# Kernel tuning notes

Measured on AMD Instinct MI355X. Metric: run time of the kernel, lower is better.

Reference implementation:

```python
import jax, jax.numpy as jnp
from jax import lax
import numpy as np

# ---- init hyperparameters (from init_kwargs) ----
STRIDE = 1
DP_CHANNELS = 1
ATOM_R = 8
ATOM_C = 8
NUMB_ATOM = 128
T_SC = 3
K = 256
BATCH = 32
IMG = 64


def setup_inputs() -> dict:
    key = jax.random.key(0)
    k1, k2 = jax.random.split(key)
    Y = jax.random.normal(k1, (BATCH, DP_CHANNELS, IMG, IMG), dtype=jnp.float32)
    # ConvTranspose2d weight layout: (numb_atom, dp_channels, atom_c, atom_r)
    W = jax.random.normal(k2, (NUMB_ATOM, DP_CHANNELS, ATOM_C, ATOM_R), dtype=jnp.float32)
    # normalise_weights(): each (i, j) filter divided by its L2 norm
    W = W / jnp.sqrt(jnp.sum(W ** 2, axis=(2, 3), keepdims=True))
    return {"Y": Y, "W_D": W}


def _conv_D(X, W):
    # PyTorch ConvTranspose2d (stride=1, no padding): full convolution with
    # spatially-flipped kernel; W is (in=numb_atom, out=dp_channels, kh, kw).
    kh, kw = W.shape[2], W.shape[3]
    return lax.conv_general_dilated(
        X, jnp.flip(W, (2, 3)), (1, 1),
        [(kh - 1, kh - 1), (kw - 1, kw - 1)],
        dimension_numbers=('NCHW', 'IOHW', 'NCHW'))


def _conv_Dt(R, Wt):
    # PyTorch Conv2d (VALID, stride=1): Wt is (out=numb_atom, in=dp, kh, kw)
    return lax.conv_general_dilated(
        R, Wt, (1, 1), 'VALID', dimension_numbers=('NCHW', 'OIHW', 'NCHW'))


def _hard_threshold_k(X, k):
    # keep the k largest-|.| entries per sample (over flattened C,H,W)
    B = X.shape[0]
    flat = X.reshape(B, -1)
    _, idx = lax.top_k(jnp.abs(flat), k)                      # [B, k]
    vals = jnp.take_along_axis(flat, idx, axis=1)             # [B, k]
    out = jnp.zeros_like(flat).at[jnp.arange(B)[:, None], idx].set(vals)
    return out.reshape(X.shape)


def _linesearch(Y, X, W, Wt, k):
    R = Y - _conv_D(X, W)
    g = _conv_Dt(R, Wt)
    l2_start = jnp.sum(R ** 2)

    def attempt(alpha):
        Xu = _hard_threshold_k(X + alpha * g, k)
        err = jnp.sum((Y - _conv_D(Xu, W)) ** 2)
        return Xu, err

    Xu0, err0 = attempt(jnp.float32(1.0))

    def cond(s):
        _, _, err, count = s
        return (err >= l2_start) & (count <= 15)

    def body(s):
        alpha, _, _, count = s
        alpha = alpha * jnp.float32(0.5)
        Xu, err = attempt(alpha)
        return (alpha, Xu, err, count + 1)

    alpha, Xu, err, _ = lax.while_loop(
        cond, body, (jnp.float32(1.0), Xu0, err0, jnp.int32(0)))
    return Xu, err, alpha


def reference(Y, W_D):
    # D_trans.weight = D.weight.permute(0,1,3,2) -> (numb_atom, dp, atom_r, atom_c)
    Wt = jnp.swapaxes(W_D, 2, 3)
    kh, kw = Wt.shape[2], Wt.shape[3]
    B, _, H, W_sp = Y.shape
    X = jnp.zeros((B, W_D.shape[0], H - kh + 1, W_sp - kw + 1), dtype=Y.dtype)
    for _ in range(T_SC):
        X, _, _ = _linesearch(Y, X, W_D, Wt, K)
    return X
```

## Files before the change

kernel.cpp:

```cpp
#include <hip/hip_runtime.h>
#include <stdint.h>

#define NB   32
#define NCH  128
#define IMG  64
#define IMG2 4096
#define OH   57
#define OHW  3249
#define CHW  415872
#define KTOP 256
#define NATT 17
#define NS   32
#define SCAP 512
#define NCAP 1536
#define NBUCK 8192
#define HSHIFT 18
#define TGT  512
#define RSTRIDE 72
#define NZB  257
#define BMW  12996

typedef unsigned long long ull;

__global__ void k_init(int* support_cnt) {
    if (threadIdx.x < NB) support_cnt[threadIdx.x] = 0;
}

__global__ __launch_bounds__(256) void k_resid(
    const float* __restrict__ Y, const float* __restrict__ W,
    const int* __restrict__ support_cnt, const uint32_t* __restrict__ support_idx,
    const float* __restrict__ support_val, float* __restrict__ Rg, double* __restrict__ l2part,
    uint32_t* __restrict__ hist, int* __restrict__ cand_cnt)
{
    int bx = blockIdx.x, tid = threadIdx.x;
    if (bx >= NB) {
        int zb = bx - NB;
        if (zb < 256) {
            ((uint4*)hist)[zb * 256 + tid] = make_uint4(0u, 0u, 0u, 0u);
        } else {
            ((uint4*)cand_cnt)[tid] = make_uint4(0u, 0u, 0u, 0u);
        }
        return;
    }
    int b = bx;
    __shared__ float Rs[IMG2];
    const float4* Y4 = (const float4*)(Y + b * IMG2);
    float4* R4 = (float4*)Rs;
    for (int i = tid; i < IMG2 / 4; i += 256) R4[i] = Y4[i];
    __syncthreads();
    int n = support_cnt[b];
    for (int task = tid; task < n * 64; task += 256) {
        int i = task >> 6, tap = task & 63, p = tap >> 3, q = tap & 7;
        uint32_t idx = support_idx[b * KTOP + i];
        float val = support_val[b * KTOP + i];
        int c = idx / OHW, rem = idx % OHW, s = rem / OH, t = rem % OH;
        float w = W[c * 64 + p * 8 + q];
        atomicAdd(&Rs[(s + p) * IMG + (t + q)], -val * w);
    }
    __syncthreads();
    double acc = 0.0;
    for (int i = tid; i < IMG2; i += 256) {
        float v = Rs[i];
        Rg[b * IMG2 + i] = v;
        acc += (double)v * (double)v;
    }
    __shared__ double red[256];
    red[tid] = acc; __syncthreads();
    for (int s2 = 128; s2 > 0; s2 >>= 1) { if (tid < s2) red[tid] += red[tid + s2]; __syncthreads(); }
    if (tid == 0) l2part[b] = red[0];
}

__global__ __launch_bounds__(256) void k_conv(
    const float* __restrict__ Rg, const float* __restrict__ W,
    float* __restrict__ g_out, uint32_t* __restrict__ hist)
{
    int b = blockIdx.x, cg0 = blockIdx.y, tid = threadIdx.x;
    __shared__ float Rs[71 * 72];
    __shared__ uint32_t hl[NBUCK];
    for (int i = tid; i < 71 * 72; i += 256) Rs[i] = 0.f;
    for (int i = tid; i < NBUCK; i += 256) hl[i] = 0u;
    __syncthreads();
    const float4* R4 = (const float4*)(Rg + b * IMG2);
    for (int i = tid; i < 1024; i += 256) {
        int row = i >> 4, col4 = (i & 15) * 4;
        *(float4*)&Rs[row * 72 + col4] = R4[i];
    }
    __syncthreads();
    int csub = tid >> 7;
    int tile = tid & 127;
    bool active = tile < 120;
    int tr = active ? tile / 15 : 0;
    int tc = active ? tile % 15 : 0;
    int s0 = tr * 8, t0 = tc * 4;

    for (int sub = 0; sub < 4; ++sub) {
        int c = cg0 * 8 + sub * 2 + csub;
        int c_s = __builtin_amdgcn_readfirstlane(c);
        const float* Wc = W + c_s * 64;

        float acc[8][4];
#pragma unroll
        for (int r = 0; r < 8; ++r)
#pragma unroll
            for (int cc = 0; cc < 4; ++cc) acc[r][cc] = 0.f;

#pragma unroll
        for (int rho = 0; rho < 15; ++rho) {
            float rb[12];
            const float* rp = &Rs[(s0 + rho) * 72 + t0];
            *(float4*)&rb[0] = *(const float4*)rp;
            *(float4*)&rb[4] = *(const float4*)(rp + 4);
            *(float4*)&rb[8] = *(const float4*)(rp + 8);
#pragma unroll
            for (int r = 0; r < 8; ++r) {
                const int p = rho - r;
                if (p >= 0 && p < 8) {
#pragma unroll
                    for (int q = 0; q < 8; ++q) {
                        float wv = Wc[q * 8 + p];
#pragma unroll
                        for (int cc = 0; cc < 4; ++cc)
                            acc[r][cc] = fmaf(rb[cc + q], wv, acc[r][cc]);
                    }
                }
            }
        }
        if (active) {
            float* go = g_out + (size_t)(b * NCH + c) * OHW;
#pragma unroll
            for (int r = 0; r < 8; ++r) {
                int s = s0 + r;
                if (s < OH) {
#pragma unroll
                    for (int cc = 0; cc < 4; ++cc) {
                        int t = t0 + cc;
                        if (t < OH) {
                            float v = acc[r][cc];
                            go[s * OH + t] = v;
                            uint32_t bits = __float_as_uint(v) & 0x7fffffffu;
                            atomicAdd(&hl[bits >> HSHIFT], 1u);
                        }
                    }
                }
            }
        }
    }
    __syncthreads();
    for (int i = tid; i < NBUCK; i += 256) {
        uint32_t v = hl[i];
        if (v) atomicAdd(&hist[b * NBUCK + i], v);
    }
}

__global__ __launch_bounds__(256) void k_thresh(const uint32_t* __restrict__ hist,
                                                uint32_t* __restrict__ thr) {
    int b = blockIdx.x, tid = threadIdx.x;
    uint32_t h[32];
    uint32_t s = 0;
    const uint32_t* hb = hist + b * NBUCK + tid * 32;
#pragma unroll
    for (int k = 0; k < 32; ++k) { h[k] = hb[k]; s += h[k]; }
    __shared__ uint32_t buf[2][256];
    int cur = 0;
    buf[0][tid] = s;
    __syncthreads();
    for (int d = 1; d < 256; d <<= 1) {
        uint32_t v = buf[cur][tid];
        if (tid + d < 256) v += buf[cur][tid + d];
        buf[cur ^ 1][tid] = v;
        cur ^= 1;
        __syncthreads();
    }
    uint32_t sufme = buf[cur][tid];
    uint32_t base  = (tid < 255) ? buf[cur][tid + 1] : 0u;
    if (tid == 0 && buf[cur][0] < TGT) thr[b] = 0u;
    if (base < TGT && sufme >= TGT) {
        uint32_t acc = base; int bk = 0;
#pragma unroll
        for (int k = 31; k >= 0; --k) {
            acc += h[k];
            if (acc >= TGT) { bk = tid * 32 + k; break; }
        }
        thr[b] = (uint32_t)bk << HSHIFT;
    }
}

__global__ __launch_bounds__(256) void k_collect(
    const float* __restrict__ g, const uint32_t* __restrict__ thr,
    int* __restrict__ cand_cnt, uint32_t* __restrict__ cand_idx, float* __restrict__ cand_g)
{
    int b = blockIdx.y;
    int i4 = blockIdx.x * 256 + threadIdx.x;
    if (i4 >= CHW / 4) return;
    int slice = blockIdx.x & (NS - 1);
    uint32_t tb = thr[b];
    float4 v4 = ((const float4*)(g + (size_t)b * CHW))[i4];
    float vv[4] = { v4.x, v4.y, v4.z, v4.w };
#pragma unroll
    for (int k = 0; k < 4; ++k) {
        uint32_t bits = __float_as_uint(vv[k]) & 0x7fffffffu;
        if (bits >= tb) {
            int pos = atomicAdd(&cand_cnt[b * NS + slice], 1);
            if (pos < SCAP) {
                cand_idx[(b * NS + slice) * SCAP + pos] = (uint32_t)(i4 * 4 + k);
                cand_g[(b * NS + slice) * SCAP + pos] = vv[k];
            }
        }
    }
}

__global__ __launch_bounds__(1024) void k_suppg(
    const float* __restrict__ g,
    const int* __restrict__ support_cnt, const uint32_t* __restrict__ support_idx,
    const int* __restrict__ cand_cnt, const uint32_t* __restrict__ cand_idx,
    const float* __restrict__ cand_g,
    uint32_t* __restrict__ ns_idx, float* __restrict__ ns_g, uint32_t* __restrict__ ns_pk,
    float* __restrict__ sup_g, uint32_t* __restrict__ sup_pk)
{
    int b = blockIdx.x, tid = threadIdx.x, lane = tid & 63;
    __shared__ uint32_t bm[BMW];
    __shared__ int cnts[NS];
    __shared__ ull ck[NCAP];
    __shared__ float cg_l[NCAP];
    __shared__ int nns_sh;
    int n = support_cnt[b];
    for (int i = tid; i < BMW / 4; i += 1024) ((uint4*)bm)[i] = make_uint4(0u, 0u, 0u, 0u);
    if (tid < NS) cnts[tid] = min(cand_cnt[b * NS + tid], SCAP);
    if (tid == 0) nns_sh = 0;
    __syncthreads();
    if (tid < KTOP) {
        if (tid < n) {
            uint32_t idx = support_idx[b * KTOP + tid];
            atomicOr(&bm[idx >> 5], 1u << (idx & 31));
            float gv = g[(size_t)b * CHW + idx];
            sup_g[b * KTOP + tid] = gv;
            int c = idx / OHW, r = idx % OHW, s = r / OH, t = r % OH;
            sup_pk[b * KTOP + tid] = (uint32_t)((c << 12) | (s << 6) | t);
        } else {
            sup_g[b * KTOP + tid] = 0.f;
            sup_pk[b * KTOP + tid] = 0u;
        }
    }
    __syncthreads();
    for (int t0 = tid; t0 < NS * SCAP; t0 += 1024) {
        int s = t0 >> 9, j = t0 & (SCAP - 1);
        bool keep = false; uint32_t idx = 0; float gv = 0.f;
        if (j < cnts[s]) {
            idx = cand_idx[(b * NS + s) * SCAP + j];
            gv = cand_g[(b * NS + s) * SCAP + j];
            keep = ((bm[idx >> 5] >> (idx & 31)) & 1u) == 0u;
        }
        ull mk = __ballot(keep);
        if (mk) {
            int basep = 0;
            if (lane == 0) basep = atomicAdd(&nns_sh, (int)__popcll(mk));
            basep = __shfl(basep, 0, 64);
            if (keep) {
                int p = basep + (int)__popcll(mk & ((1ull << lane) - 1ull));
                if (p < NCAP) {
                    ck[p] = ((ull)(__float_as_uint(gv) & 0x7fffffffu) << 32) | (ull)(uint32_t)(~idx);
                    cg_l[p] = gv;
                }
            }
        }
    }
    __syncthreads();
    int nns = min(nns_sh, NCAP);
    ull myk[2]; int myr[2];
#pragma unroll
    for (int q = 0; q < 2; ++q) { int i = tid + 1024 * q; myk[q] = (i < nns) ? ck[i] : 0ull; myr[q] = 0; }
    for (int j = 0; j < nns; ++j) {
        ull kj = ck[j];
#pragma unroll
        for (int q = 0; q < 2; ++q) myr[q] += (kj > myk[q]) ? 1 : 0;
    }
#pragma unroll
    for (int q = 0; q < 2; ++q) {
        int i = tid + 1024 * q;
        if (i < nns && myr[q] < KTOP) {
            uint32_t idx = ~(uint32_t)myk[q];
            int r = myr[q];
            ns_idx[b * KTOP + r] = idx;
            ns_g[b * KTOP + r] = cg_l[i];
            int c = idx / OHW, rr = idx % OHW, s = rr / OH, t = rr % OH;
            ns_pk[b * KTOP + r] = (uint32_t)((c << 12) | (s << 6) | t);
        }
    }
}

__global__ __launch_bounds__(256) void k_sel(
    const int* __restrict__ support_cnt, const uint32_t* __restrict__ support_idx,
    const float* __restrict__ support_val,
    const float* __restrict__ sup_g, const uint32_t* __restrict__ sup_pk,
    const uint32_t* __restrict__ ns_idx, const float* __restrict__ ns_g,
    const uint32_t* __restrict__ ns_pk,
    uint32_t* __restrict__ sel_idx, float* __restrict__ sel_val, uint32_t* __restrict__ sel_pk)
{
    int a = blockIdx.x, b = blockIdx.y, tid = threadIdx.x;
    float alpha = ldexpf(1.f, -a);
    int n = support_cnt[b];

    __shared__ ull ku[512];
    __shared__ uint32_t s_ci[KTOP];
    __shared__ float s_v[KTOP];
    __shared__ uint32_t s_pk[KTOP];

    uint32_t nsi = ns_idx[b * KTOP + tid];
    float v_ns = alpha * ns_g[b * KTOP + tid];
    uint32_t pk_ns = ns_pk[b * KTOP + tid];
    ull k_ns = ((ull)(__float_as_uint(v_ns) & 0x7fffffffu) << 32) | (ull)(uint32_t)(~nsi);
    ku[tid] = k_ns;
    uint32_t spi; float v_sup; uint32_t pk_sup;
    if (tid < n) {
        spi = support_idx[b * KTOP + tid];
        v_sup = fmaf(alpha, sup_g[b * KTOP + tid], support_val[b * KTOP + tid]);
        pk_sup = sup_pk[b * KTOP + tid];
    } else {
        spi = (uint32_t)(CHW + tid);
        v_sup = 0.f; pk_sup = 0u;
    }
    ull k_sup = ((ull)(__float_as_uint(v_sup) & 0x7fffffffu) << 32) | (ull)(uint32_t)(~spi);
    ku[256 + tid] = k_sup;
    __syncthreads();

    int c_ns = 0, c_sup = 0;
    for (int j = 0; j < 512; ++j) {
        ull kj = ku[j];
        c_ns += (kj > k_ns) ? 1 : 0;
        c_sup += (kj > k_sup) ? 1 : 0;
    }
    if (c_ns < KTOP) { s_ci[c_ns] = nsi; s_v[c_ns] = v_ns; s_pk[c_ns] = pk_ns; }
    if (c_sup < KTOP) { s_ci[c_sup] = spi; s_v[c_sup] = v_sup; s_pk[c_sup] = pk_sup; }
    __syncthreads();

    size_t o = ((size_t)a * NB + b) * KTOP + tid;
    sel_idx[o] = s_ci[tid];
    sel_val[o] = s_v[tid];
    sel_pk[o] = s_pk[tid];
}

__global__ __launch_bounds__(1024) void k_err(
    const float* __restrict__ Y, const float* __restrict__ W,
    const float* __restrict__ sel_val, const uint32_t* __restrict__ sel_pk,
    double* __restrict__ err)
{
    int a = blockIdx.x, b = blockIdx.y, tid = threadIdx.x;
    int lane = tid & 63, wid = tid >> 6;
    __shared__ float recon[64 * RSTRIDE];
    __shared__ float s_v[KTOP];
    __shared__ uint32_t s_pk[KTOP];
    __shared__ double redd[16];

    for (int i = tid; i < 64 * RSTRIDE; i += 1024) recon[i] = 0.f;
    if (tid < KTOP) {
        size_t o = ((size_t)a * NB + b) * KTOP + tid;
        s_v[tid] = sel_val[o];
        s_pk[tid] = sel_pk[o];
    }
    __syncthreads();
    for (int task = tid; task < KTOP * 64; task += 1024) {
        int i = task >> 6, tap = task & 63, p = tap >> 3, q = tap & 7;
        uint32_t pk = s_pk[i];
        float val = s_v[i];
        int c = pk >> 12, s = (pk >> 6) & 63, t = pk & 63;
        atomicAdd(&recon[(s + p) * RSTRIDE + (t + q)], val * W[c * 64 + tap]);
    }
    __syncthreads();
    float4 y4 = ((const float4*)(Y + b * IMG2))[tid];
    int row = tid >> 4, col = (tid & 15) * 4;
    const float* rr = &recon[row * RSTRIDE + col];
    double accd = 0.0;
    float d0 = y4.x - rr[0]; accd += (double)d0 * (double)d0;
    float d1 = y4.y - rr[1]; accd += (double)d1 * (double)d1;
    float d2 = y4.z - rr[2]; accd += (double)d2 * (double)d2;
    float d3 = y4.w - rr[3]; accd += (double)d3 * (double)d3;
    for (int d = 32; d > 0; d >>= 1) accd += __shfl_xor(accd, d, 64);
    if (lane == 0) redd[wid] = accd;
    __syncthreads();
    if (tid == 0) {
        double e = 0.0;
#pragma unroll
        for (int w2 = 0; w2 < 16; ++w2) e += redd[w2];
        err[a * NB + b] = e;
    }
}

__global__ __launch_bounds__(256) void k_update(
    const double* __restrict__ l2part, const double* __restrict__ err,
    const uint32_t* __restrict__ sel_idx, const float* __restrict__ sel_val,
    int* __restrict__ support_cnt, uint32_t* __restrict__ support_idx, float* __restrict__ support_val)
{
    int b = blockIdx.x, tid = threadIdx.x;
    __shared__ double esum[NATT + 1];
    __shared__ int sel_sh;
    if (tid < NATT) {
        double e = 0.0;
        for (int b2 = 0; b2 < NB; ++b2) e += err[tid * NB + b2];
        esum[tid] = e;
    } else if (tid == NATT) {
        double l2 = 0.0;
        for (int b2 = 0; b2 < NB; ++b2) l2 += l2part[b2];
        esum[NATT] = l2;
    }
    __syncthreads();
    if (tid == 0) {
        double l2 = esum[NATT];
        int sel = NATT - 1;
        for (int a2 = 0; a2 < NATT; ++a2) if (esum[a2] < l2) { sel = a2; break; }
        sel_sh = sel;
    }
    __syncthreads();
    int a = sel_sh;
    __shared__ uint32_t ki[KTOP];
    __shared__ float kv[KTOP];
    ki[tid] = sel_idx[((size_t)a * NB + b) * KTOP + tid];
    kv[tid] = sel_val[((size_t)a * NB + b) * KTOP + tid];
    __syncthreads();
    uint32_t me = ki[tid];
    int rank = 0;
    for (int j = 0; j < KTOP; ++j) rank += (ki[j] < me) ? 1 : 0;
    support_idx[b * KTOP + rank] = me;
    support_val[b * KTOP + rank] = kv[tid];
    if (tid == 0) support_cnt[b] = KTOP;
}

__global__ void k_outzero(float4* __restrict__ out) {
    int i = blockIdx.x * 256 + threadIdx.x;
    if (i < (NB * CHW) / 4) out[i] = make_float4(0.f, 0.f, 0.f, 0.f);
}

__global__ void k_scatter(const uint32_t* __restrict__ support_idx, const float* __restrict__ support_val,
                          float* __restrict__ out) {
    int b = blockIdx.x, tid = threadIdx.x;
    if (tid < KTOP) out[(size_t)b * CHW + support_idx[b * KTOP + tid]] = support_val[b * KTOP + tid];
}

static size_t align256(size_t x) { return (x + 255) & ~(size_t)255; }

extern "C" void kernel_launch(void* const* d_in, const int* in_sizes, int n_in,
                              void* d_out, int out_size, void* d_ws, size_t ws_size,
                              hipStream_t stream)
{
    const float* Y = (const float*)d_in[0];
    const float* W = (const float*)d_in[1];
    float* out = (float*)d_out;

    char* p = (char*)d_ws;
    size_t off = 0;
    auto carve = [&](size_t bytes) { void* r = p + off; off = align256(off + bytes); return r; };
    float*    Rg          = (float*)   carve(NB * IMG2 * sizeof(float));
    uint32_t* hist        = (uint32_t*)carve((size_t)NB * NBUCK * sizeof(uint32_t));
    uint32_t* thr         = (uint32_t*)carve(NB * sizeof(uint32_t));
    int*      cand_cnt    = (int*)     carve(NB * NS * sizeof(int));
    double*   l2part      = (double*)  carve(NB * sizeof(double));
    double*   err         = (double*)  carve(NATT * NB * sizeof(double));
    int*      support_cnt = (int*)     carve(NB * sizeof(int));
    uint32_t* support_idx = (uint32_t*)carve(NB * KTOP * sizeof(uint32_t));
    float*    support_val = (float*)   carve(NB * KTOP * sizeof(float));
    uint32_t* sel_idx     = (uint32_t*)carve((size_t)NATT * NB * KTOP * sizeof(uint32_t));
    float*    sel_val     = (float*)   carve((size_t)NATT * NB * KTOP * sizeof(float));
    uint32_t* sel_pk      = (uint32_t*)carve((size_t)NATT * NB * KTOP * sizeof(uint32_t));
    uint32_t* cand_idx    = (uint32_t*)carve((size_t)NB * NS * SCAP * sizeof(uint32_t));
    float*    cand_g      = (float*)   carve((size_t)NB * NS * SCAP * sizeof(float));
    uint32_t* ns_idx      = (uint32_t*)carve(NB * KTOP * sizeof(uint32_t));
    float*    ns_gbuf     = (float*)   carve(NB * KTOP * sizeof(float));
    uint32_t* ns_pk       = (uint32_t*)carve(NB * KTOP * sizeof(uint32_t));
    float*    sup_gbuf    = (float*)   carve(NB * KTOP * sizeof(float));
    uint32_t* sup_pk      = (uint32_t*)carve(NB * KTOP * sizeof(uint32_t));
    (void)ws_size; (void)in_sizes; (void)n_in; (void)out_size;

    k_init<<<1, 64, 0, stream>>>(support_cnt);
    for (int t = 0; t < 3; ++t) {
        k_resid<<<NB + NZB, 256, 0, stream>>>(Y, W, support_cnt, support_idx, support_val,
                                              Rg, l2part, hist, cand_cnt);
        k_conv<<<dim3(NB, 16), 256, 0, stream>>>(Rg, W, out, hist);
        k_thresh<<<NB, 256, 0, stream>>>(hist, thr);
        k_collect<<<dim3((CHW / 4 + 255) / 256, NB), 256, 0, stream>>>(out, thr, cand_cnt, cand_idx, cand_g);
        k_suppg<<<NB, 1024, 0, stream>>>(out, support_cnt, support_idx,
                                         cand_cnt, cand_idx, cand_g,
                                         ns_idx, ns_gbuf, ns_pk, sup_gbuf, sup_pk);
        k_sel<<<dim3(NATT, NB), 256, 0, stream>>>(support_cnt, support_idx, support_val,
                                                  sup_gbuf, sup_pk, ns_idx, ns_gbuf, ns_pk,
                                                  sel_idx, sel_val, sel_pk);
        k_err<<<dim3(NATT, NB), 1024, 0, stream>>>(Y, W, sel_val, sel_pk, err);
        k_update<<<NB, 256, 0, stream>>>(l2part, err, sel_idx, sel_val,
                                         support_cnt, support_idx, support_val);
    }
    k_outzero<<<((NB * CHW) / 4 + 255) / 256, 256, 0, stream>>>((float4*)out);
    k_scatter<<<NB, 256, 0, stream>>>(support_idx, support_val, out);
}
```

Baseline: 695.6 us.

## Fuse selection and error kernels, merge-rank sorted lists, stage weights in LDS

Merges k_sel and k_err into one 1024-thread kernel per (attempt, batch). Four waves rank the candidates by merging two lists that are already sorted (binary search plus a count against the other list), while the remaining waves zero the recon buffer and stage W into shared memory. This removes a kernel launch, the global round trip of sel_pk, and the global W reads inside the atomic scatter loop. Several O(n^2) rank loops are also unrolled by 8; the cost is higher LDS use and the assumption that both input lists are already sorted by key.

```diff
diff --git a/kernel.cpp b/kernel.cpp
--- a/kernel.cpp
+++ b/kernel.cpp
@@ -266,13 +266,22 @@
     }
     __syncthreads();
     int nns = min(nns_sh, NCAP);
+    int nns8 = (nns + 7) & ~7;
+    for (int i = nns + tid; i < nns8; i += 1024) ck[i] = 0ull;
+    __syncthreads();
     ull myk[2]; int myr[2];
 #pragma unroll
     for (int q = 0; q < 2; ++q) { int i = tid + 1024 * q; myk[q] = (i < nns) ? ck[i] : 0ull; myr[q] = 0; }
-    for (int j = 0; j < nns; ++j) {
-        ull kj = ck[j];
-#pragma unroll
-        for (int q = 0; q < 2; ++q) myr[q] += (kj > myk[q]) ? 1 : 0;
+    for (int j = 0; j < nns8; j += 8) {
+        ull t0 = ck[j], t1 = ck[j+1], t2 = ck[j+2], t3 = ck[j+3];
+        ull t4 = ck[j+4], t5 = ck[j+5], t6 = ck[j+6], t7 = ck[j+7];
+#pragma unroll
+        for (int q = 0; q < 2; ++q) {
+            myr[q] += ((t0 > myk[q]) ? 1 : 0) + ((t1 > myk[q]) ? 1 : 0)
+                    + ((t2 > myk[q]) ? 1 : 0) + ((t3 > myk[q]) ? 1 : 0)
+                    + ((t4 > myk[q]) ? 1 : 0) + ((t5 > myk[q]) ? 1 : 0)
+                    + ((t6 > myk[q]) ? 1 : 0) + ((t7 > myk[q]) ? 1 : 0);
+        }
     }
 #pragma unroll
     for (int q = 0; q < 2; ++q) {
@@ -288,84 +297,93 @@
     }
 }
 
-__global__ __launch_bounds__(256) void k_sel(
+__global__ __launch_bounds__(1024) void k_att2(
+    const float* __restrict__ Y, const float* __restrict__ W,
     const int* __restrict__ support_cnt, const uint32_t* __restrict__ support_idx,
     const float* __restrict__ support_val,
     const float* __restrict__ sup_g, const uint32_t* __restrict__ sup_pk,
     const uint32_t* __restrict__ ns_idx, const float* __restrict__ ns_g,
     const uint32_t* __restrict__ ns_pk,
-    uint32_t* __restrict__ sel_idx, float* __restrict__ sel_val, uint32_t* __restrict__ sel_pk)
+    uint32_t* __restrict__ sel_idx, float* __restrict__ sel_val, double* __restrict__ err)
 {
     int a = blockIdx.x, b = blockIdx.y, tid = threadIdx.x;
+    int lane = tid & 63, wid = tid >> 6;
     float alpha = ldexpf(1.f, -a);
     int n = support_cnt[b];
 
-    __shared__ ull ku[512];
-    __shared__ uint32_t s_ci[KTOP];
+    __shared__ float Wlds[NCH * 64];
+    __shared__ float recon[64 * RSTRIDE];
+    __shared__ ull kA[KTOP];
+    __shared__ ull kB[KTOP];
     __shared__ float s_v[KTOP];
-    __shared__ uint32_t s_pk[KTOP];
-
-    uint32_t nsi = ns_idx[b * KTOP + tid];
-    float v_ns = alpha * ns_g[b * KTOP + tid];
-    uint32_t pk_ns = ns_pk[b * KTOP + tid];
-    ull k_ns = ((ull)(__float_as_uint(v_ns) & 0x7fffffffu) << 32) | (ull)(uint32_t)(~nsi);
-    ku[tid] = k_ns;
-    uint32_t spi; float v_sup; uint32_t pk_sup;
-    if (tid < n) {
-        spi = support_idx[b * KTOP + tid];
-        v_sup = fmaf(alpha, sup_g[b * KTOP + tid], support_val[b * KTOP + tid]);
-        pk_sup = sup_pk[b * KTOP + tid];
+    __shared__ uint32_t s_pk2[KTOP];
+    __shared__ double redd[16];
+
+    uint32_t nsi = 0, pk_ns = 0, spi = 0, pk_sup = 0;
+    float v_ns = 0.f, v_sup = 0.f;
+    ull k_ns = 0, k_sup = 0;
+    if (wid < 4) {
+        nsi = ns_idx[b * KTOP + tid];
+        v_ns = alpha * ns_g[b * KTOP + tid];
+        pk_ns = ns_pk[b * KTOP + tid];
+        k_ns = ((ull)(__float_as_uint(v_ns) & 0x7fffffffu) << 32) | (ull)(uint32_t)(~nsi);
+        kA[tid] = k_ns;
+        if (tid < n) {
+            spi = support_idx[b * KTOP + tid];
+            v_sup = fmaf(alpha, sup_g[b * KTOP + tid], support_val[b * KTOP + tid]);
+            pk_sup = sup_pk[b * KTOP + tid];
+        } else {
+            spi = (uint32_t)(CHW + tid);
+            v_sup = 0.f; pk_sup = 0u;
+        }
+        k_sup = ((ull)(__float_as_uint(v_sup) & 0x7fffffffu) << 32) | (ull)(uint32_t)(~spi);
+        kB[tid] = k_sup;
+    }
+    __syncthreads();
+
+    if (wid < 4) {
+        int cb_ns = 0, cb_sup = 0;
+        for (int j = 0; j < KTOP; j += 8) {
+            ull t0 = kB[j], t1 = kB[j+1], t2 = kB[j+2], t3 = kB[j+3];
+            ull t4 = kB[j+4], t5 = kB[j+5], t6 = kB[j+6], t7 = kB[j+7];
+            cb_ns  += ((t0 > k_ns) ? 1 : 0) + ((t1 > k_ns) ? 1 : 0)
+                    + ((t2 > k_ns) ? 1 : 0) + ((t3 > k_ns) ? 1 : 0)
+                    + ((t4 > k_ns) ? 1 : 0) + ((t5 > k_ns) ? 1 : 0)
+                    + ((t6 > k_ns) ? 1 : 0) + ((t7 > k_ns) ? 1 : 0);
+            cb_sup += ((t0 > k_sup) ? 1 : 0) + ((t1 > k_sup) ? 1 : 0)
+                    + ((t2 > k_sup) ? 1 : 0) + ((t3 > k_sup) ? 1 : 0)
+                    + ((t4 > k_sup) ? 1 : 0) + ((t5 > k_sup) ? 1 : 0)
+                    + ((t6 > k_sup) ? 1 : 0) + ((t7 > k_sup) ? 1 : 0);
+        }
+        int rank_ns = tid + cb_ns;
+        int lo = 0, hi = KTOP;
+        while (lo < hi) { int mid = (lo + hi) >> 1; if (kA[mid] > k_sup) lo = mid + 1; else hi = mid; }
+        int rank_sup = lo + cb_sup;
+        size_t o = ((size_t)a * NB + b) * KTOP;
+        if (rank_ns < KTOP) {
+            s_v[rank_ns] = v_ns; s_pk2[rank_ns] = pk_ns;
+            sel_idx[o + rank_ns] = nsi; sel_val[o + rank_ns] = v_ns;
+        }
+        if (rank_sup < KTOP) {
+            s_v[rank_sup] = v_sup; s_pk2[rank_sup] = pk_sup;
+            sel_idx[o + rank_sup] = spi; sel_val[o + rank_sup] = v_sup;
+        }
     } else {
-        spi = (uint32_t)(CHW + tid);
-        v_sup = 0.f; pk_sup = 0u;
-    }
-    ull k_sup = ((ull)(__float_as_uint(v_sup) & 0x7fffffffu) << 32) | (ull)(uint32_t)(~spi);
-    ku[256 + tid] = k_sup;
-    __syncthreads();
-
-    int c_ns = 0, c_sup = 0;
-    for (int j = 0; j < 512; ++j) {
-        ull kj = ku[j];
-        c_ns += (kj > k_ns) ? 1 : 0;
-        c_sup += (kj > k_sup) ? 1 : 0;
-    }
-    if (c_ns < KTOP) { s_ci[c_ns] = nsi; s_v[c_ns] = v_ns; s_pk[c_ns] = pk_ns; }
-    if (c_sup < KTOP) { s_ci[c_sup] = spi; s_v[c_sup] = v_sup; s_pk[c_sup] = pk_sup; }
-    __syncthreads();
-
-    size_t o = ((size_t)a * NB + b) * KTOP + tid;
-    sel_idx[o] = s_ci[tid];
-    sel_val[o] = s_v[tid];
-    sel_pk[o] = s_pk[tid];
-}
-
-__global__ __launch_bounds__(1024) void k_err(
-    const float* __restrict__ Y, const float* __restrict__ W,
-    const float* __restrict__ sel_val, const uint32_t* __restrict__ sel_pk,
-    double* __restrict__ err)
-{
-    int a = blockIdx.x, b = blockIdx.y, tid = threadIdx.x;
-    int lane = tid & 63, wid = tid >> 6;
-    __shared__ float recon[64 * RSTRIDE];
-    __shared__ float s_v[KTOP];
-    __shared__ uint32_t s_pk[KTOP];
-    __shared__ double redd[16];
-
-    for (int i = tid; i < 64 * RSTRIDE; i += 1024) recon[i] = 0.f;
-    if (tid < KTOP) {
-        size_t o = ((size_t)a * NB + b) * KTOP + tid;
-        s_v[tid] = sel_val[o];
-        s_pk[tid] = sel_pk[o];
-    }
-    __syncthreads();
+        for (int i = tid - 256; i < 64 * RSTRIDE; i += 768) recon[i] = 0.f;
+        for (int i = tid - 256; i < (NCH * 64) / 4; i += 768)
+            ((float4*)Wlds)[i] = ((const float4*)W)[i];
+    }
+    __syncthreads();
+
     for (int task = tid; task < KTOP * 64; task += 1024) {
         int i = task >> 6, tap = task & 63, p = tap >> 3, q = tap & 7;
-        uint32_t pk = s_pk[i];
+        uint32_t pk = s_pk2[i];
         float val = s_v[i];
         int c = pk >> 12, s = (pk >> 6) & 63, t = pk & 63;
-        atomicAdd(&recon[(s + p) * RSTRIDE + (t + q)], val * W[c * 64 + tap]);
-    }
-    __syncthreads();
+        atomicAdd(&recon[(s + p) * RSTRIDE + (t + q)], val * Wlds[c * 64 + tap]);
+    }
+    __syncthreads();
+
     float4 y4 = ((const float4*)(Y + b * IMG2))[tid];
     int row = tid >> 4, col = (tid & 15) * 4;
     const float* rr = &recon[row * RSTRIDE + col];
@@ -418,7 +436,12 @@
     __syncthreads();
     uint32_t me = ki[tid];
     int rank = 0;
-    for (int j = 0; j < KTOP; ++j) rank += (ki[j] < me) ? 1 : 0;
+    for (int j = 0; j < KTOP; j += 8) {
+        uint32_t a0 = ki[j], a1 = ki[j+1], a2 = ki[j+2], a3 = ki[j+3];
+        uint32_t a4 = ki[j+4], a5 = ki[j+5], a6 = ki[j+6], a7 = ki[j+7];
+        rank += ((a0 < me) ? 1 : 0) + ((a1 < me) ? 1 : 0) + ((a2 < me) ? 1 : 0) + ((a3 < me) ? 1 : 0)
+              + ((a4 < me) ? 1 : 0) + ((a5 < me) ? 1 : 0) + ((a6 < me) ? 1 : 0) + ((a7 < me) ? 1 : 0);
+    }
     support_idx[b * KTOP + rank] = me;
     support_val[b * KTOP + rank] = kv[tid];
     if (tid == 0) support_cnt[b] = KTOP;
@@ -459,7 +482,6 @@
     float*    support_val = (float*)   carve(NB * KTOP * sizeof(float));
     uint32_t* sel_idx     = (uint32_t*)carve((size_t)NATT * NB * KTOP * sizeof(uint32_t));
     float*    sel_val     = (float*)   carve((size_t)NATT * NB * KTOP * sizeof(float));
-    uint32_t* sel_pk      = (uint32_t*)carve((size_t)NATT * NB * KTOP * sizeof(uint32_t));
     uint32_t* cand_idx    = (uint32_t*)carve((size_t)NB * NS * SCAP * sizeof(uint32_t));
     float*    cand_g      = (float*)   carve((size_t)NB * NS * SCAP * sizeof(float));
     uint32_t* ns_idx      = (uint32_t*)carve(NB * KTOP * sizeof(uint32_t));
@@ -479,10 +501,9 @@
         k_suppg<<<NB, 1024, 0, stream>>>(out, support_cnt, support_idx,
                                          cand_cnt, cand_idx, cand_g,
                                          ns_idx, ns_gbuf, ns_pk, sup_gbuf, sup_pk);
-        k_sel<<<dim3(NATT, NB), 256, 0, stream>>>(support_cnt, support_idx, support_val,
-                                                  sup_gbuf, sup_pk, ns_idx, ns_gbuf, ns_pk,
-                                                  sel_idx, sel_val, sel_pk);
-        k_err<<<dim3(NATT, NB), 1024, 0, stream>>>(Y, W, sel_val, sel_pk, err);
+        k_att2<<<dim3(NATT, NB), 1024, 0, stream>>>(Y, W, support_cnt, support_idx, support_val,
+                                                    sup_gbuf, sup_pk, ns_idx, ns_gbuf, ns_pk,
+                                                    sel_idx, sel_val, err);
         k_update<<<NB, 256, 0, stream>>>(l2part, err, sel_idx, sel_val,
                                          support_cnt, support_idx, support_val);
     }
```

Result: faster. 671.0 us (-3.5%).
